# Optimization experiments

Hardware: AMD Instinct MI355X
Metric: run time of the kernel (lower is better)

## Reference

```python
import jax, jax.numpy as jnp
import numpy as np

B, S, D, H = 4, 1024, 1024, 16
HD = D // H
EPS = 1e-5


def _layernorm(x, g, b):
    m = jnp.mean(x, axis=-1, keepdims=True)
    v = jnp.mean((x - m) ** 2, axis=-1, keepdims=True)
    return (x - m) * jax.lax.rsqrt(v + EPS) * g + b


def setup_inputs() -> dict:
    key = jax.random.key(0)
    ks = jax.random.split(key, 8)
    sc = 1.0 / np.sqrt(D)
    return {
        "x": jax.random.normal(ks[0], (B, S, D), dtype=jnp.float32),
        "seq_len": jax.random.randint(ks[1], (B,), 1, S + 1, dtype=jnp.int32),
        "Wq": jax.random.normal(ks[2], (D, D), dtype=jnp.float32) * sc,
        "bq": jnp.zeros((D,), dtype=jnp.float32),
        "Wk": jax.random.normal(ks[3], (D, D), dtype=jnp.float32) * sc,
        "bk": jnp.zeros((D,), dtype=jnp.float32),
        "Wv": jax.random.normal(ks[4], (D, D), dtype=jnp.float32) * sc,
        "bv": jnp.zeros((D,), dtype=jnp.float32),
        "ln_g": jnp.ones((HD,), dtype=jnp.float32),
        "ln_b": jnp.zeros((HD,), dtype=jnp.float32),
    }


def reference(x, seq_len, Wq, bq, Wk, bk, Wv, bv, ln_g, ln_b):
    # Faithful quirk: k and v are projections of the ALREADY projected q.
    q = x @ Wq.T + bq                      # [B,S,D]
    k = q @ Wk.T + bk
    v = q @ Wv.T + bv
    # [B,S,D] -> [B,H,S,HD]
    def split_heads(t):
        return t.reshape(B, S, H, HD).transpose(0, 2, 1, 3)
    q, k, v = split_heads(q), split_heads(k), split_heads(v)
    # shared per-head LayerNorm over head_dim
    q = _layernorm(q, ln_g, ln_b)
    k = _layernorm(k, ln_g, ln_b)
    v = _layernorm(v, ln_g, ln_b)
    # raw scores (no temperature scaling in the original; temperature=1.0 unused)
    scores = jnp.einsum("bhqd,bhkd->bhqk", q, k)
    # encoder_mask: multiplicative validity mask on key positions, repeated per head
    mask = (jnp.arange(S)[None, :] < seq_len[:, None]).astype(scores.dtype)  # [B,S]
    scores = scores * mask[:, None, None, :]
    attn = jax.nn.softmax(scores, axis=-1)
    # dropout is identity at inference
    out = jnp.einsum("bhqk,bhkd->bhqd", attn, v)
    return out.transpose(0, 2, 1, 3).reshape(B, S, D)
```

## Files before the change

kernel.cpp:

```cpp
#include <hip/hip_runtime.h>

#define B_  4
#define S_  1024
#define D_  1024
#define H_  16
#define HD_ 64
#define EPS_ 1e-5f

typedef _Float16 f16x8 __attribute__((ext_vector_type(8)));
typedef _Float16 f16x4 __attribute__((ext_vector_type(4)));
typedef __bf16 bf16x8 __attribute__((ext_vector_type(8)));
typedef float  f32x4  __attribute__((ext_vector_type(4)));
typedef unsigned short ushort8v __attribute__((ext_vector_type(8)));

static __device__ __forceinline__ unsigned short f2bf(float f) {
  union { float f; unsigned u; } v; v.f = f;
  unsigned r = v.u + 0x7fffu + ((v.u >> 16) & 1u);
  return (unsigned short)(r >> 16);
}
static __device__ __forceinline__ float bf2f(unsigned short u) {
  union { unsigned u; float f; } v; v.u = ((unsigned)u) << 16;
  return v.f;
}

#define GLD16(gp, lp) __builtin_amdgcn_global_load_lds( \
    (const __attribute__((address_space(1))) void*)(gp), \
    (__attribute__((address_space(3))) void*)(lp), 16, 0, 0)

__global__ __launch_bounds__(256) void cvt_all(
    const float* __restrict__ x,  _Float16* __restrict__ xh,
    const float* __restrict__ Wq, _Float16* __restrict__ wqh,
    const float* __restrict__ Wk, _Float16* __restrict__ wkh,
    const float* __restrict__ Wv, _Float16* __restrict__ wvh,
    float* __restrict__ Vtail) {
  int bid = blockIdx.x;
  if (bid >= 7168) {
    int i = (bid - 7168) * 1024 + threadIdx.x * 4;
    *(float4*)(Vtail + i) = make_float4(0.f, 0.f, 0.f, 0.f);
    return;
  }
  const float* src; _Float16* dst; int base;
  if (bid < 4096)      { src = x;  dst = xh;  base = bid; }
  else if (bid < 5120) { src = Wq; dst = wqh; base = bid - 4096; }
  else if (bid < 6144) { src = Wk; dst = wkh; base = bid - 5120; }
  else                 { src = Wv; dst = wvh; base = bid - 6144; }
  int i = base * 1024 + threadIdx.x * 4;
  float4 f = *(const float4*)(src + i);
  f16x4 h;
  h.x = (_Float16)f.x; h.y = (_Float16)f.y; h.z = (_Float16)f.z; h.w = (_Float16)f.w;
  *(f16x4*)(dst + i) = h;
}

__global__ __launch_bounds__(256, 2) void gemm_bt_bias(
    const _Float16* __restrict__ A,
    const _Float16* __restrict__ B0, const float* __restrict__ bias0,
    _Float16* __restrict__ C0,
    const _Float16* __restrict__ B1, const float* __restrict__ bias1,
    _Float16* __restrict__ C1,
    int M, int N, int K)
{
  const _Float16* Bm = blockIdx.z ? B1 : B0;
  const float* bias  = blockIdx.z ? bias1 : bias0;
  _Float16* C        = blockIdx.z ? C1 : C0;

  __shared__ _Float16 As[2 * 128 * 32];
  __shared__ _Float16 Bs[2 * 64 * 32];

  int tid  = threadIdx.x;
  int lane = tid & 63;
  int wave = tid >> 6;
  int wm = wave >> 1, wn = wave & 1;
  int qd = lane >> 4, l15 = lane & 15;

  long row0 = (long)blockIdx.y * 128;
  long col0 = (long)blockIdx.x * 64;

  int r_a = tid >> 2;
  int c_a = (tid & 3) * 8;

  f32x4 acc[4][2] = {};

  for (int kk = 0; kk < K; kk += 64) {
    GLD16(A  + (row0 + r_a) * K + kk + c_a,           As + tid * 8);
    GLD16(A  + (row0 + 64 + r_a) * K + kk + c_a,      As + 2048 + tid * 8);
    GLD16(A  + (row0 + r_a) * K + kk + 32 + c_a,      As + 4096 + tid * 8);
    GLD16(A  + (row0 + 64 + r_a) * K + kk + 32 + c_a, As + 6144 + tid * 8);
    GLD16(Bm + (col0 + r_a) * K + kk + c_a,           Bs + tid * 8);
    GLD16(Bm + (col0 + r_a) * K + kk + 32 + c_a,      Bs + 2048 + tid * 8);
    __syncthreads();

    for (int ks = 0; ks < 2; ks++) {
      f16x8 af[4], bfr[2];
      for (int t = 0; t < 4; t++)
        af[t]  = *(const f16x8*)(As + ks * 4096 + (wm * 64 + t * 16 + l15) * 32 + qd * 8);
      for (int j = 0; j < 2; j++)
        bfr[j] = *(const f16x8*)(Bs + ks * 2048 + (wn * 32 + j * 16 + l15) * 32 + qd * 8);
      for (int i = 0; i < 4; i++)
        for (int j = 0; j < 2; j++)
          acc[i][j] = __builtin_amdgcn_mfma_f32_16x16x32_f16(af[i], bfr[j], acc[i][j], 0, 0, 0);
    }
    __syncthreads();
  }

  for (int i = 0; i < 4; i++) {
    long row = row0 + wm * 64 + i * 16 + qd * 4;
    for (int j = 0; j < 2; j++) {
      long col = col0 + wn * 32 + j * 16 + l15;
      float bv = bias[col];
      for (int r = 0; r < 4; r++)
        C[(row + r) * N + col] = (_Float16)(acc[i][j][r] + bv);
    }
  }
}

__global__ __launch_bounds__(256, 2) void gemm_bt_bias128(
    const _Float16* __restrict__ A,
    const _Float16* __restrict__ B0, const float* __restrict__ bias0,
    _Float16* __restrict__ C0,
    const _Float16* __restrict__ B1, const float* __restrict__ bias1,
    _Float16* __restrict__ C1,
    int M, int N, int K)
{
  const _Float16* Bm = blockIdx.z ? B1 : B0;
  const float* bias  = blockIdx.z ? bias1 : bias0;
  _Float16* C        = blockIdx.z ? C1 : C0;

  __shared__ _Float16 As[2 * 128 * 32];
  __shared__ _Float16 Bs[2 * 128 * 32];

  int tid  = threadIdx.x;
  int lane = tid & 63;
  int wave = tid >> 6;
  int wm = wave >> 1, wn = wave & 1;
  int qd = lane >> 4, l15 = lane & 15;

  long row0 = (long)blockIdx.y * 128;
  long col0 = (long)blockIdx.x * 128;

  int r_a = tid >> 2;
  int c_a = (tid & 3) * 8;

  f32x4 acc[4][4] = {};

  for (int kk = 0; kk < K; kk += 64) {
    GLD16(A  + (row0 + r_a) * K + kk + c_a,           As + tid * 8);
    GLD16(A  + (row0 + 64 + r_a) * K + kk + c_a,      As + 2048 + tid * 8);
    GLD16(A  + (row0 + r_a) * K + kk + 32 + c_a,      As + 4096 + tid * 8);
    GLD16(A  + (row0 + 64 + r_a) * K + kk + 32 + c_a, As + 6144 + tid * 8);
    GLD16(Bm + (col0 + r_a) * K + kk + c_a,           Bs + tid * 8);
    GLD16(Bm + (col0 + 64 + r_a) * K + kk + c_a,      Bs + 2048 + tid * 8);
    GLD16(Bm + (col0 + r_a) * K + kk + 32 + c_a,      Bs + 4096 + tid * 8);
    GLD16(Bm + (col0 + 64 + r_a) * K + kk + 32 + c_a, Bs + 6144 + tid * 8);
    __syncthreads();

    for (int ks = 0; ks < 2; ks++) {
      f16x8 af[4], bfr[4];
      for (int t = 0; t < 4; t++) {
        af[t]  = *(const f16x8*)(As + ks * 4096 + (wm * 64 + t * 16 + l15) * 32 + qd * 8);
        bfr[t] = *(const f16x8*)(Bs + ks * 4096 + (wn * 64 + t * 16 + l15) * 32 + qd * 8);
      }
      for (int i = 0; i < 4; i++)
        for (int j = 0; j < 4; j++)
          acc[i][j] = __builtin_amdgcn_mfma_f32_16x16x32_f16(af[i], bfr[j], acc[i][j], 0, 0, 0);
    }
    __syncthreads();
  }

  for (int i = 0; i < 4; i++) {
    long row = row0 + wm * 64 + i * 16 + qd * 4;
    for (int j = 0; j < 4; j++) {
      long col = col0 + wn * 64 + j * 16 + l15;
      float bv = bias[col];
      for (int r = 0; r < 4; r++)
        C[(row + r) * N + col] = (_Float16)(acc[i][j][r] + bv);
    }
  }
}

__global__ __launch_bounds__(256) void ln_qkv(
    const _Float16* __restrict__ qh,
    const _Float16* __restrict__ kh,
    const _Float16* __restrict__ vh,
    const float* __restrict__ ln_g, const float* __restrict__ ln_b,
    const int* __restrict__ seq_len,
    _Float16* __restrict__ Qn,
    _Float16* __restrict__ Kn,
    unsigned short* __restrict__ Vt,
    float* __restrict__ Vtail)
{
  __shared__ unsigned short Vls[256][68];
  int tid = threadIdx.x;
  int s0 = blockIdx.x * 256;
  int h = blockIdx.y, b = blockIdx.z;
  long bh = (long)b * H_ + h;
  long s = s0 + tid;
  long inbase  = ((long)b * S_ + s) * D_ + (long)h * HD_;
  long outbase = (bh * S_ + s) * HD_;

  f16x8 rq[8], rk[8], rv[8];
  for (int i = 0; i < 8; i++) {
    rq[i] = *(const f16x8*)(qh + inbase + i * 8);
    rk[i] = *(const f16x8*)(kh + inbase + i * 8);
    rv[i] = *(const f16x8*)(vh + inbase + i * 8);
  }

  {
    float sum = 0.f, sq = 0.f;
    for (int i = 0; i < 8; i++)
      for (int j = 0; j < 8; j++) { float xv = (float)rq[i][j]; sum += xv; sq = fmaf(xv, xv, sq); }
    float m = sum * (1.f / 64.f);
    float inv = rsqrtf(sq * (1.f / 64.f) - m * m + EPS_);
    for (int i = 0; i < 8; i++) {
      f16x8 o;
      for (int j = 0; j < 8; j++)
        o[j] = (_Float16)(((float)rq[i][j] - m) * inv * ln_g[i * 8 + j] + ln_b[i * 8 + j]);
      *(f16x8*)(Qn + outbase + i * 8) = o;
    }
  }
  {
    float sum = 0.f, sq = 0.f;
    for (int i = 0; i < 8; i++)
      for (int j = 0; j < 8; j++) { float xv = (float)rk[i][j]; sum += xv; sq = fmaf(xv, xv, sq); }
    float m = sum * (1.f / 64.f);
    float inv = rsqrtf(sq * (1.f / 64.f) - m * m + EPS_);
    for (int i = 0; i < 8; i++) {
      f16x8 o;
      for (int j = 0; j < 8; j++)
        o[j] = (_Float16)(((float)rk[i][j] - m) * inv * ln_g[i * 8 + j] + ln_b[i * 8 + j]);
      *(f16x8*)(Kn + outbase + i * 8) = o;
    }
  }
  {
    float sum = 0.f, sq = 0.f;
    for (int i = 0; i < 8; i++)
      for (int j = 0; j < 8; j++) { float xv = (float)rv[i][j]; sum += xv; sq = fmaf(xv, xv, sq); }
    float m = sum * (1.f / 64.f);
    float inv = rsqrtf(sq * (1.f / 64.f) - m * m + EPS_);
    for (int i = 0; i < 8; i++)
      for (int j = 0; j < 8; j++)
        Vls[tid][i * 8 + j] = f2bf(((float)rv[i][j] - m) * inv * ln_g[i * 8 + j] + ln_b[i * 8 + j]);
  }
  __syncthreads();
  int d = tid >> 2, sc = tid & 3;
  int len = seq_len[b];
  long vbase = (bh * HD_ + d) * S_ + s0 + sc * 64;
  float tsum = 0.f;
  for (int j0 = 0; j0 < 64; j0 += 8) {
    ushort8v w;
    for (int jj = 0; jj < 8; jj++) {
      unsigned short ub = Vls[sc * 64 + j0 + jj][d];
      w[jj] = ub;
      if (s0 + sc * 64 + j0 + jj >= len) tsum += bf2f(ub);
    }
    *(ushort8v*)(Vt + vbase + j0) = w;
  }
  if (s0 + sc * 64 + 64 > len)
    atomicAdd(&Vtail[bh * HD_ + d], tsum);
}

__global__ __launch_bounds__(256, 2) void attn(
    const _Float16* __restrict__ Qn,
    const _Float16* __restrict__ Kn,
    const unsigned short* __restrict__ Vt,
    const float* __restrict__ Vtail,
    const int* __restrict__ seq_len,
    float* __restrict__ out)
{
  __shared__ _Float16 Ks[2][64 * 32];
  __shared__ unsigned short Vts[2][64 * 32];
  __shared__ unsigned short Ps[4][32 * 72];

  int tid = threadIdx.x, lane = tid & 63, wave = tid >> 6;
  int qd = lane >> 4, l15 = lane & 15;
  int b = blockIdx.x;
  int h = blockIdx.y;
  int q0 = blockIdx.z * 128;
  long bh = (long)b * H_ + h;
  int len = seq_len[b];
  int ntile = (len + 63) >> 6;

  int skey = tid >> 2;
  int schunk = (tid & 3) * 8;

  f16x8 qf[2][2];
  for (int mt = 0; mt < 2; mt++) {
    const _Float16* qp = Qn + (bh * S_ + q0 + wave * 32 + mt * 16 + l15) * HD_;
    qf[mt][0] = *(const f16x8*)(qp + qd * 8);
    qf[mt][1] = *(const f16x8*)(qp + 32 + qd * 8);
  }
  float tv[4];
  for (int t = 0; t < 4; t++) tv[t] = Vtail[bh * HD_ + t * 16 + l15];

  f32x4 o[2][4] = {};
  float den[2][4] = {{0.f,0.f,0.f,0.f},{0.f,0.f,0.f,0.f}};

  for (int kt = 0; kt < ntile; kt++) {
    GLD16(Kn + (bh * S_ + kt * 64 + skey) * HD_ + schunk,      &Ks[0][0] + tid * 8);
    GLD16(Kn + (bh * S_ + kt * 64 + skey) * HD_ + 32 + schunk, &Ks[1][0] + tid * 8);
    GLD16(Vt + (bh * HD_ + skey) * S_ + kt * 64 + schunk,      &Vts[0][0] + tid * 8);
    GLD16(Vt + (bh * HD_ + skey) * S_ + kt * 64 + 32 + schunk, &Vts[1][0] + tid * 8);
    __syncthreads();

    f32x4 sacc[2][4] = {};
    for (int tn = 0; tn < 4; tn++) {
      f16x8 kf0 = *(const f16x8*)(&Ks[0][0] + (tn * 16 + l15) * 32 + qd * 8);
      f16x8 kf1 = *(const f16x8*)(&Ks[1][0] + (tn * 16 + l15) * 32 + qd * 8);
      for (int mt = 0; mt < 2; mt++) {
        sacc[mt][tn] = __builtin_amdgcn_mfma_f32_16x16x32_f16(qf[mt][0], kf0, sacc[mt][tn], 0, 0, 0);
        sacc[mt][tn] = __builtin_amdgcn_mfma_f32_16x16x32_f16(qf[mt][1], kf1, sacc[mt][tn], 0, 0, 0);
      }
    }

    for (int mt = 0; mt < 2; mt++)
      for (int tn = 0; tn < 4; tn++) {
        int kg = kt * 64 + tn * 16 + l15;
        for (int r = 0; r < 4; r++) {
          float p = (kg < len) ? __expf(sacc[mt][tn][r]) : 0.f;
          unsigned short pb = f2bf(p);
          den[mt][r] += bf2f(pb);
          Ps[wave][(mt * 16 + qd * 4 + r) * 72 + tn * 16 + l15] = pb;
        }
      }

    bf16x8 pf[2][2];
    for (int mt = 0; mt < 2; mt++) {
      pf[mt][0] = *(const bf16x8*)(&Ps[wave][(mt * 16 + l15) * 72 + qd * 8]);
      pf[mt][1] = *(const bf16x8*)(&Ps[wave][(mt * 16 + l15) * 72 + 32 + qd * 8]);
    }
    for (int t = 0; t < 4; t++) {
      bf16x8 vf0 = *(const bf16x8*)(&Vts[0][0] + (t * 16 + l15) * 32 + qd * 8);
      bf16x8 vf1 = *(const bf16x8*)(&Vts[1][0] + (t * 16 + l15) * 32 + qd * 8);
      for (int mt = 0; mt < 2; mt++) {
        o[mt][t] = __builtin_amdgcn_mfma_f32_16x16x32_bf16(pf[mt][0], vf0, o[mt][t], 0, 0, 0);
        o[mt][t] = __builtin_amdgcn_mfma_f32_16x16x32_bf16(pf[mt][1], vf1, o[mt][t], 0, 0, 0);
      }
    }
    __syncthreads();
  }

  for (int mt = 0; mt < 2; mt++)
    for (int t = 0; t < 4; t++)
      for (int r = 0; r < 4; r++) o[mt][t][r] += tv[t];

  float tden = (float)(S_ - len);
  for (int mt = 0; mt < 2; mt++)
    for (int r = 0; r < 4; r++) {
      for (int off = 1; off < 16; off <<= 1)
        den[mt][r] += __shfl_xor(den[mt][r], off, 64);
      den[mt][r] += tden;
    }

  for (int mt = 0; mt < 2; mt++)
    for (int t = 0; t < 4; t++)
      for (int r = 0; r < 4; r++) {
        long s = q0 + wave * 32 + mt * 16 + qd * 4 + r;
        long dcol = (long)h * HD_ + t * 16 + l15;
        out[((long)b * S_ + s) * D_ + dcol] = o[mt][t][r] / den[mt][r];
      }
}

extern "C" void kernel_launch(void* const* d_in, const int* in_sizes, int n_in,
                              void* d_out, int out_size, void* d_ws, size_t ws_size,
                              hipStream_t stream) {
  const float* x     = (const float*)d_in[0];
  const int*  seq    = (const int*)d_in[1];
  const float* Wq    = (const float*)d_in[2];
  const float* bq    = (const float*)d_in[3];
  const float* Wk    = (const float*)d_in[4];
  const float* bk    = (const float*)d_in[5];
  const float* Wv    = (const float*)d_in[6];
  const float* bv    = (const float*)d_in[7];
  const float* ln_g  = (const float*)d_in[8];
  const float* ln_b  = (const float*)d_in[9];
  float* out = (float*)d_out;

  char* ws = (char*)d_ws;
  _Float16* xh  = (_Float16*)(ws);
  _Float16* wqh = (_Float16*)(ws + (8l  << 20));
  _Float16* wkh = (_Float16*)(ws + (10l << 20));
  _Float16* wvh = (_Float16*)(ws + (12l << 20));
  float*    Vtail = (float*)(ws + (14l << 20));
  _Float16* qh  = (_Float16*)(ws + (16l << 20));
  _Float16* kh  = (_Float16*)(ws + (24l << 20));
  _Float16* vh  = (_Float16*)(ws + (32l << 20));
  _Float16* Qn  = (_Float16*)(ws + (40l << 20));
  _Float16* Kn  = (_Float16*)(ws + (48l << 20));
  unsigned short* Vt = (unsigned short*)(ws + (56l << 20));

  cvt_all<<<7172, 256, 0, stream>>>(x, xh, Wq, wqh, Wk, wkh, Wv, wvh, Vtail);

  dim3 g1(D_ / 64, (B_ * S_) / 128, 1);
  gemm_bt_bias<<<g1, 256, 0, stream>>>(xh, wqh, bq, qh, wqh, bq, qh,
                                       B_ * S_, D_, D_);
  dim3 g2(D_ / 128, (B_ * S_) / 128, 2);
  gemm_bt_bias128<<<g2, 256, 0, stream>>>(qh, wkh, bk, kh, wvh, bv, vh,
                                          B_ * S_, D_, D_);

  dim3 g3(S_ / 256, H_, B_);
  ln_qkv<<<g3, 256, 0, stream>>>(qh, kh, vh, ln_g, ln_b, seq, Qn, Kn, Vt, Vtail);

  dim3 g4(B_, H_, S_ / 128);
  attn<<<g4, 256, 0, stream>>>(Qn, Kn, Vt, Vtail, seq, out);
}
```

Baseline: 181.2 us.

## Double-buffer K/V tiles in attention loop and split full/partial tile softmax

Adds a second LDS buffer for K and V tiles so the next tile's global-to-LDS loads are issued before computing on the current tile, aiming to hide load latency behind the MFMA work. The exp/bf16 conversion loop also gets a fast path with no per-key validity check for tiles fully below seq_len. This doubles K/V LDS usage, which could limit occupancy at 2 blocks per CU. It also depends on the single end-of-iteration barrier ordering correctly with the async loads (GLD16 semantics).

```diff
diff --git a/kernel.cpp b/kernel.cpp
--- a/kernel.cpp
+++ b/kernel.cpp
@@ -266,8 +266,8 @@
     const int* __restrict__ seq_len,
     float* __restrict__ out)
 {
-  __shared__ _Float16 Ks[2][64 * 32];
-  __shared__ unsigned short Vts[2][64 * 32];
+  __shared__ _Float16 Ks[2][2][64 * 32];
+  __shared__ unsigned short Vts[2][2][64 * 32];
   __shared__ unsigned short Ps[4][32 * 72];
 
   int tid = threadIdx.x, lane = tid & 63, wave = tid >> 6;
@@ -294,33 +294,59 @@
   f32x4 o[2][4] = {};
   float den[2][4] = {{0.f,0.f,0.f,0.f},{0.f,0.f,0.f,0.f}};
 
+  const _Float16* kp       = Kn + (bh * S_ + skey) * HD_ + schunk;
+  const unsigned short* vp = Vt + (bh * HD_ + skey) * S_ + schunk;
+
+  GLD16(kp,      &Ks[0][0][0]  + tid * 8);
+  GLD16(kp + 32, &Ks[0][1][0]  + tid * 8);
+  GLD16(vp,      &Vts[0][0][0] + tid * 8);
+  GLD16(vp + 32, &Vts[0][1][0] + tid * 8);
+  __syncthreads();
+
   for (int kt = 0; kt < ntile; kt++) {
-    GLD16(Kn + (bh * S_ + kt * 64 + skey) * HD_ + schunk,      &Ks[0][0] + tid * 8);
-    GLD16(Kn + (bh * S_ + kt * 64 + skey) * HD_ + 32 + schunk, &Ks[1][0] + tid * 8);
-    GLD16(Vt + (bh * HD_ + skey) * S_ + kt * 64 + schunk,      &Vts[0][0] + tid * 8);
-    GLD16(Vt + (bh * HD_ + skey) * S_ + kt * 64 + 32 + schunk, &Vts[1][0] + tid * 8);
-    __syncthreads();
+    int cur = kt & 1, nxt = cur ^ 1;
+
+    if (kt + 1 < ntile) {
+      long koff = (long)(kt + 1) * 64 * HD_;
+      long voff = (long)(kt + 1) * 64;
+      GLD16(kp + koff,      &Ks[nxt][0][0]  + tid * 8);
+      GLD16(kp + koff + 32, &Ks[nxt][1][0]  + tid * 8);
+      GLD16(vp + voff,      &Vts[nxt][0][0] + tid * 8);
+      GLD16(vp + voff + 32, &Vts[nxt][1][0] + tid * 8);
+    }
 
     f32x4 sacc[2][4] = {};
     for (int tn = 0; tn < 4; tn++) {
-      f16x8 kf0 = *(const f16x8*)(&Ks[0][0] + (tn * 16 + l15) * 32 + qd * 8);
-      f16x8 kf1 = *(const f16x8*)(&Ks[1][0] + (tn * 16 + l15) * 32 + qd * 8);
+      f16x8 kf0 = *(const f16x8*)(&Ks[cur][0][0] + (tn * 16 + l15) * 32 + qd * 8);
+      f16x8 kf1 = *(const f16x8*)(&Ks[cur][1][0] + (tn * 16 + l15) * 32 + qd * 8);
       for (int mt = 0; mt < 2; mt++) {
         sacc[mt][tn] = __builtin_amdgcn_mfma_f32_16x16x32_f16(qf[mt][0], kf0, sacc[mt][tn], 0, 0, 0);
         sacc[mt][tn] = __builtin_amdgcn_mfma_f32_16x16x32_f16(qf[mt][1], kf1, sacc[mt][tn], 0, 0, 0);
       }
     }
 
-    for (int mt = 0; mt < 2; mt++)
-      for (int tn = 0; tn < 4; tn++) {
-        int kg = kt * 64 + tn * 16 + l15;
-        for (int r = 0; r < 4; r++) {
-          float p = (kg < len) ? __expf(sacc[mt][tn][r]) : 0.f;
-          unsigned short pb = f2bf(p);
-          den[mt][r] += bf2f(pb);
-          Ps[wave][(mt * 16 + qd * 4 + r) * 72 + tn * 16 + l15] = pb;
+    if (kt * 64 + 64 <= len) {
+      for (int mt = 0; mt < 2; mt++)
+        for (int tn = 0; tn < 4; tn++)
+          for (int r = 0; r < 4; r++) {
+            float p = __expf(sacc[mt][tn][r]);
+            unsigned short pb = f2bf(p);
+            den[mt][r] += bf2f(pb);
+            Ps[wave][(mt * 16 + qd * 4 + r) * 72 + tn * 16 + l15] = pb;
+          }
+    } else {
+      for (int mt = 0; mt < 2; mt++)
+        for (int tn = 0; tn < 4; tn++) {
+          int kg = kt * 64 + tn * 16 + l15;
+          bool valid = kg < len;
+          for (int r = 0; r < 4; r++) {
+            float p = valid ? __expf(sacc[mt][tn][r]) : 0.f;
+            unsigned short pb = f2bf(p);
+            den[mt][r] += bf2f(pb);
+            Ps[wave][(mt * 16 + qd * 4 + r) * 72 + tn * 16 + l15] = pb;
+          }
         }
-      }
+    }
 
     bf16x8 pf[2][2];
     for (int mt = 0; mt < 2; mt++) {
@@ -328,13 +354,14 @@
       pf[mt][1] = *(const bf16x8*)(&Ps[wave][(mt * 16 + l15) * 72 + 32 + qd * 8]);
     }
     for (int t = 0; t < 4; t++) {
-      bf16x8 vf0 = *(const bf16x8*)(&Vts[0][0] + (t * 16 + l15) * 32 + qd * 8);
-      bf16x8 vf1 = *(const bf16x8*)(&Vts[1][0] + (t * 16 + l15) * 32 + qd * 8);
+      bf16x8 vf0 = *(const bf16x8*)(&Vts[cur][0][0] + (t * 16 + l15) * 32 + qd * 8);
+      bf16x8 vf1 = *(const bf16x8*)(&Vts[cur][1][0] + (t * 16 + l15) * 32 + qd * 8);
       for (int mt = 0; mt < 2; mt++) {
         o[mt][t] = __builtin_amdgcn_mfma_f32_16x16x32_bf16(pf[mt][0], vf0, o[mt][t], 0, 0, 0);
         o[mt][t] = __builtin_amdgcn_mfma_f32_16x16x32_bf16(pf[mt][1], vf1, o[mt][t], 0, 0, 0);
       }
     }
+
     __syncthreads();
   }
 
```

After: 182.7 us. Within noise of the previous version (+0.8%).
